# Performance work log

Hardware: AMD Instinct MI355X
Metric: run time of the kernel (lower is better)

The kernel has to match this reference:

```python
import jax, jax.numpy as jnp
import numpy as np

D_MODEL = 1024
N_HEADS = 16
HEAD_D = D_MODEL // N_HEADS  # d_keys == d_values == 64
B, L = 4, 2048
EPS_CAUSAL = 1e-6


def setup_inputs() -> dict:
    key = jax.random.key(0)
    ks = jax.random.split(key, 11)
    s = 1.0 / np.sqrt(D_MODEL)
    inp = {
        "queries": jax.random.normal(ks[0], (B, L, D_MODEL), jnp.float32),
        "keys": jax.random.normal(ks[1], (B, L, D_MODEL), jnp.float32),
        "values": jax.random.normal(ks[2], (B, L, D_MODEL), jnp.float32),
        # Linear weights stored as [in, out] so y = x @ W + b (same math as torch Linear)
        "Wq": jax.random.uniform(ks[3], (D_MODEL, N_HEADS * HEAD_D), jnp.float32, -s, s),
        "bq": jax.random.uniform(ks[4], (N_HEADS * HEAD_D,), jnp.float32, -s, s),
        "Wk": jax.random.uniform(ks[5], (D_MODEL, N_HEADS * HEAD_D), jnp.float32, -s, s),
        "bk": jax.random.uniform(ks[6], (N_HEADS * HEAD_D,), jnp.float32, -s, s),
        "Wv": jax.random.uniform(ks[7], (D_MODEL, N_HEADS * HEAD_D), jnp.float32, -s, s),
        "bv": jax.random.uniform(ks[8], (N_HEADS * HEAD_D,), jnp.float32, -s, s),
        "Wo": jax.random.uniform(ks[9], (D_MODEL, D_MODEL), jnp.float32, -s, s),
        "bo": jax.random.uniform(ks[10], (D_MODEL,), jnp.float32, -s, s),
    }
    return inp


def _feat(x):
    # feat_proj: elu(x) + 1
    return jax.nn.elu(x) + 1.0


def _causal_linear_attn(qs, ks, vs):
    # qs/ks: [B,L,H,D], vs: [B,L,H,K]; faithful to original (swapped einsum labels,
    # elementwise denominator).
    def step(carry, xs):
        Si, Zi = carry  # Si: [B,H,D,K], Zi: [B,H,D]
        q, k, v = xs    # each [B,H,D]
        Si = Si + jnp.einsum('bhd,bhk->bhdk', k, v)
        Zi = Zi + k
        num = jnp.einsum('bhd,bhkd->bhk', q, Si)      # note label swap, as in source
        Vi = num / (q * Zi + EPS_CAUSAL)               # elementwise denom, as in source
        return (Si, Zi), Vi

    Bn, Ln, H, D = qs.shape
    K = vs.shape[-1]
    Si0 = jnp.zeros((Bn, H, D, K), qs.dtype)
    Zi0 = jnp.zeros((Bn, H, D), qs.dtype)
    xs = (jnp.swapaxes(qs, 0, 1), jnp.swapaxes(ks, 0, 1), jnp.swapaxes(vs, 0, 1))
    _, out = jax.lax.scan(step, (Si0, Zi0), xs)  # out: [L,B,H,K]
    return jnp.swapaxes(out, 0, 1)               # [B,L,H,K]


def reference(queries, keys, values, Wq, bq, Wk, bk, Wv, bv, Wo, bo):
    N, Lq, _ = queries.shape
    H = N_HEADS
    Q = (queries @ Wq + bq).reshape(N, Lq, H, -1)
    Kp = (keys @ Wk + bk).reshape(N, keys.shape[1], H, -1)
    V = (values @ Wv + bv).reshape(N, values.shape[1], H, -1)
    Q_lin = _feat(Q)
    K_lin = _feat(Kp)
    V_lin = _causal_linear_attn(Q_lin, K_lin, V)  # causal=True branch
    new_values = V_lin.reshape(N, Lq, -1)
    return new_values @ Wo + bo
```

## Files before the change

### kernel.cpp

```cpp
#include <hip/hip_runtime.h>
#include <math.h>

#define DM 1024
#define LL 2048
#define BB 4
#define HH 16
#define HD 64
#define CC 64
#define NC (LL / CC)
#define EPSC 1e-6f
#define PS 72

typedef __attribute__((ext_vector_type(8))) short short8;
typedef __attribute__((ext_vector_type(4))) float floatx4;

__device__ __forceinline__ float featf(float x) { return x > 0.f ? x + 1.f : __expf(x); }

__device__ __forceinline__ unsigned short f2bf(float f) {
    unsigned int u = __builtin_bit_cast(unsigned int, f);
    u = (u + 0x7FFFu + ((u >> 16) & 1u)) >> 16;
    return (unsigned short)u;
}
__device__ __forceinline__ float bf2f(unsigned short h) {
    return __builtin_bit_cast(float, (unsigned int)h << 16);
}
__device__ __forceinline__ void split2(float f, unsigned short& h, unsigned short& l) {
    h = f2bf(f);
    l = f2bf(f - bf2f(h));
}

__device__ __forceinline__ void gload_lds16(const void* g, void* l) {
    __builtin_amdgcn_global_load_lds(
        (const __attribute__((address_space(1))) void*)g,
        (__attribute__((address_space(3))) void*)l,
        16, 0, 0);
}

__global__ __launch_bounds__(256) void convert3(
    const float* __restrict__ a, const float* __restrict__ b,
    const float* __restrict__ c, unsigned short* __restrict__ oa,
    unsigned short* __restrict__ ob, unsigned short* __restrict__ oc)
{
    const int blk = blockIdx.x;
    const int sel = blk >> 12;
    const float* src = (sel == 0) ? a : (sel == 1) ? b : c;
    unsigned short* dst = (sel == 0) ? oa : (sel == 1) ? ob : oc;
    const int i = (blk & 4095) * 256 + threadIdx.x;
    const float4 x = ((const float4*)src)[i * 2];
    const float4 y = ((const float4*)src)[i * 2 + 1];
    union { unsigned short s[8]; uint4 v; } o;
    o.s[0] = f2bf(x.x); o.s[1] = f2bf(x.y); o.s[2] = f2bf(x.z); o.s[3] = f2bf(x.w);
    o.s[4] = f2bf(y.x); o.s[5] = f2bf(y.y); o.s[6] = f2bf(y.z); o.s[7] = f2bf(y.w);
    ((uint4*)dst)[i] = o.v;
}

__global__ __launch_bounds__(256) void transpose4(
    const float* __restrict__ W0, const float* __restrict__ W1,
    const float* __restrict__ W2, const float* __restrict__ W3,
    unsigned short* __restrict__ T0, unsigned short* __restrict__ T1,
    unsigned short* __restrict__ T2, unsigned short* __restrict__ T3)
{
    __shared__ float tile[64][65];
    const int sel = blockIdx.z;
    const float* W = (sel == 0) ? W0 : (sel == 1) ? W1 : (sel == 2) ? W2 : W3;
    unsigned short* Wt = (sel == 0) ? T0 : (sel == 1) ? T1 : (sel == 2) ? T2 : T3;
    const int r0 = blockIdx.y * 64, c0 = blockIdx.x * 64;
    const int tid = threadIdx.x;
#pragma unroll
    for (int e = 0; e < 16; ++e) {
        const int idx = e * 256 + tid;
        const int r = idx >> 6, c = idx & 63;
        tile[r][c] = W[(size_t)(r0 + r) * DM + c0 + c];
    }
    __syncthreads();
#pragma unroll
    for (int e = 0; e < 16; ++e) {
        const int idx = e * 256 + tid;
        const int co = idx >> 6, ro = idx & 63;
        Wt[(size_t)(c0 + co) * DM + r0 + ro] = f2bf(tile[ro][co]);
    }
}

__global__ __launch_bounds__(256) void gemm_mfma(
    const unsigned short* __restrict__ X,
    const unsigned short* __restrict__ Wt,
    const float* __restrict__ bias,
    float* __restrict__ Y, int act, int layout)
{
    __shared__ __align__(16) unsigned short As[128 * 32];
    __shared__ __align__(16) unsigned short Bs[128 * 32];

    const int tid = threadIdx.x;
    const int lane = tid & 63;
    const int w = tid >> 6;
    const int wr = w >> 1, wc = w & 1;
    const int fm = lane & 15;
    const int fq = lane >> 4;
    const int m0 = blockIdx.y * 128, n0 = blockIdx.x * 128;

    floatx4 acc[4][4];
#pragma unroll
    for (int i = 0; i < 4; ++i)
#pragma unroll
        for (int j = 0; j < 4; ++j) acc[i][j] = (floatx4){0.f, 0.f, 0.f, 0.f};

    const int row0 = tid >> 2;
    const int row1 = row0 + 64;
    const int slot0 = (tid & 3) ^ (row0 & 3);
    const int slot1 = (tid & 3) ^ (row1 & 3);
    const unsigned short* Xa = X + (size_t)(m0 + row0) * DM + slot0 * 8;
    const unsigned short* Xb = X + (size_t)(m0 + row1) * DM + slot1 * 8;
    const unsigned short* Wa = Wt + (size_t)(n0 + row0) * DM + slot0 * 8;
    const unsigned short* Wb = Wt + (size_t)(n0 + row1) * DM + slot1 * 8;

    const int fswz = ((fq ^ (fm & 3)) << 3);

    for (int k0 = 0; k0 < DM; k0 += 32) {
        gload_lds16(Xa + k0, As + (size_t)tid * 8);
        gload_lds16(Xb + k0, As + (size_t)(256 + tid) * 8);
        gload_lds16(Wa + k0, Bs + (size_t)tid * 8);
        gload_lds16(Wb + k0, Bs + (size_t)(256 + tid) * 8);
        __syncthreads();

        short8 af[4], bf[4];
#pragma unroll
        for (int mt = 0; mt < 4; ++mt)
            af[mt] = *(const short8*)(As + (wr * 64 + mt * 16 + fm) * 32 + fswz);
#pragma unroll
        for (int nt = 0; nt < 4; ++nt)
            bf[nt] = *(const short8*)(Bs + (wc * 64 + nt * 16 + fm) * 32 + fswz);
#pragma unroll
        for (int mt = 0; mt < 4; ++mt)
#pragma unroll
            for (int nt = 0; nt < 4; ++nt)
                acc[mt][nt] = __builtin_amdgcn_mfma_f32_16x16x32_bf16(
                    af[mt], bf[nt], acc[mt][nt], 0, 0, 0);
        __syncthreads();
    }

    if (layout == 0) {
#pragma unroll
        for (int nt = 0; nt < 4; ++nt) {
            const int col = n0 + wc * 64 + nt * 16 + fm;
            const float bv = bias[col];
#pragma unroll
            for (int mt = 0; mt < 4; ++mt) {
                const int rbase = m0 + wr * 64 + mt * 16 + fq * 4;
#pragma unroll
                for (int r = 0; r < 4; ++r) {
                    float v = acc[mt][nt][r] + bv;
                    if (act) v = featf(v);
                    Y[(size_t)(rbase + r) * DM + col] = v;
                }
            }
        }
    } else {
        const int b = m0 >> 11;
        const int cch = ((m0 & 2047) >> 6) + wr;
        const int h = (n0 >> 6) + wc;
        float* base = Y + ((size_t)((b * 16 + h) * 32 + cch)) * 4096;
#pragma unroll
        for (int nt = 0; nt < 4; ++nt) {
            const int j = nt * 16 + fm;
            const float bv = bias[n0 + wc * 64 + nt * 16 + fm];
#pragma unroll
            for (int mt = 0; mt < 4; ++mt) {
                float4 o;
                o.x = acc[mt][nt][0] + bv; o.y = acc[mt][nt][1] + bv;
                o.z = acc[mt][nt][2] + bv; o.w = acc[mt][nt][3] + bv;
                if (act) { o.x = featf(o.x); o.y = featf(o.y);
                           o.z = featf(o.z); o.w = featf(o.w); }
                *(float4*)(base + j * 64 + mt * 16 + fq * 4) = o;
            }
        }
    }
}

__global__ __launch_bounds__(256) void chunk_state(
    const float* __restrict__ Kc, const float* __restrict__ Vf,
    float* __restrict__ Mstates, float* __restrict__ Zc)
{
    __shared__ __align__(16) char smem[37888];
    unsigned short* KTH = (unsigned short*)(smem);
    unsigned short* KTL = (unsigned short*)(smem + 9216);
    unsigned short* VTH = (unsigned short*)(smem + 18432);
    unsigned short* VTL = (unsigned short*)(smem + 27648);
    float* scratch = (float*)(smem + 36864);

    const int blk = blockIdx.x;
    const int bh = blk / NC, c = blk % NC;
    const int b = bh / HH, h = bh % HH;
    const int tid = threadIdx.x;
    const int w = tid >> 6;
    const int lane = tid & 63;
    const int fm = lane & 15, fq = lane >> 4;
    const size_t gbase = ((size_t)(b * LL + c * CC)) * DM + h * HD;
    const float* Kblk = Kc + (size_t)blk * 4096;

    const int lr = tid >> 2, lc0 = (tid & 3) * 16;

    {
        float ka[16];
#pragma unroll
        for (int g = 0; g < 4; ++g)
            *(float4*)(ka + g * 4) = *(const float4*)(Kblk + lr * 64 + lc0 + g * 4);
        union { unsigned short s[16]; uint4 v[2]; } hh, ll;
#pragma unroll
        for (int e = 0; e < 16; ++e) split2(ka[e], hh.s[e], ll.s[e]);
        *(uint4*)(KTH + lr * PS + lc0) = hh.v[0];
        *(uint4*)(KTH + lr * PS + lc0 + 8) = hh.v[1];
        *(uint4*)(KTL + lr * PS + lc0) = ll.v[0];
        *(uint4*)(KTL + lr * PS + lc0 + 8) = ll.v[1];
    }
    {
        float va[16];
#pragma unroll
        for (int g = 0; g < 4; ++g)
            *(float4*)(va + g * 4) = *(const float4*)(Vf + gbase + (size_t)lr * DM + lc0 + g * 4);
#pragma unroll
        for (int g = 0; g < 4; ++g)
#pragma unroll
            for (int e0 = 0; e0 < 4; ++e0) {
                const int e = g * 4 + ((e0 + tid) & 3);
                unsigned short hh, ll;
                split2(va[e], hh, ll);
                VTH[(lc0 + e) * PS + lr] = hh;
                VTL[(lc0 + e) * PS + lr] = ll;
            }
    }
    {
        const int zj = tid & 63, zs = tid >> 6;
        float z = 0.f;
#pragma unroll
        for (int g = 0; g < 4; ++g) {
            float4 kv = *(const float4*)(Kblk + zj * 64 + zs * 16 + g * 4);
            z += kv.x + kv.y + kv.z + kv.w;
        }
        scratch[zs * 64 + zj] = z;
    }
    __syncthreads();

    if (tid < 64) {
        Zc[(size_t)blk * 64 + tid] = scratch[tid] + scratch[64 + tid] +
                                     scratch[128 + tid] + scratch[192 + tid];
    }

    floatx4 acc[4];
#pragma unroll
    for (int nt = 0; nt < 4; ++nt) acc[nt] = (floatx4){0.f, 0.f, 0.f, 0.f};
    short8 aH[2], aL[2];
#pragma unroll
    for (int ks = 0; ks < 2; ++ks) {
        aH[ks] = *(const short8*)(KTH + (16 * w + fm) * PS + ks * 32 + fq * 8);
        aL[ks] = *(const short8*)(KTL + (16 * w + fm) * PS + ks * 32 + fq * 8);
    }
#pragma unroll
    for (int nt = 0; nt < 4; ++nt) {
#pragma unroll
        for (int ks = 0; ks < 2; ++ks) {
            short8 bH = *(const short8*)(VTH + (nt * 16 + fm) * PS + ks * 32 + fq * 8);
            short8 bL = *(const short8*)(VTL + (nt * 16 + fm) * PS + ks * 32 + fq * 8);
            acc[nt] = __builtin_amdgcn_mfma_f32_16x16x32_bf16(aH[ks], bH, acc[nt], 0, 0, 0);
            acc[nt] = __builtin_amdgcn_mfma_f32_16x16x32_bf16(aH[ks], bL, acc[nt], 0, 0, 0);
            acc[nt] = __builtin_amdgcn_mfma_f32_16x16x32_bf16(aL[ks], bH, acc[nt], 0, 0, 0);
        }
    }
    float* Mout = Mstates + (size_t)blk * 4096;
#pragma unroll
    for (int nt = 0; nt < 4; ++nt) {
        const int dv = nt * 16 + fm;
#pragma unroll
        for (int r = 0; r < 4; ++r) {
            const int j = 16 * w + fq * 4 + r;
            Mout[j * 64 + dv] = acc[nt][r];
        }
    }
}

__global__ __launch_bounds__(256) void prefix_state(
    float* __restrict__ Mstates, float* __restrict__ Zc)
{
    const int bh = blockIdx.x >> 4;
    const int slice = blockIdx.x & 15;
    const int off = slice * 256 + threadIdx.x;
    float run = 0.f;
    float* base = Mstates + (size_t)bh * NC * 4096 + off;
    for (int c = 0; c < NC; ++c) {
        const float v = base[(size_t)c * 4096];
        base[(size_t)c * 4096] = run;
        run += v;
    }
    if (slice == 0 && threadIdx.x < 64) {
        float z = 0.f;
        float* zb = Zc + (size_t)bh * NC * 64 + threadIdx.x;
        for (int c = 0; c < NC; ++c) {
            const float v = zb[c * 64];
            zb[c * 64] = z;
            z += v;
        }
    }
}

__global__ __launch_bounds__(256) void chunk_attn(
    const float* __restrict__ Qf, const float* __restrict__ Kc,
    const float* __restrict__ Vf, const float* __restrict__ Mprev,
    const float* __restrict__ Zprev, unsigned short* __restrict__ Outb)
{
    __shared__ __align__(16) char smem[72704];
    unsigned short* VH  = (unsigned short*)(smem);
    unsigned short* VL  = (unsigned short*)(smem + 9216);
    unsigned short* KTH = (unsigned short*)(smem + 18432);
    unsigned short* KTL = (unsigned short*)(smem + 27648);
    unsigned short* AH  = (unsigned short*)(smem + 36864);
    unsigned short* AL  = (unsigned short*)(smem + 46080);
    float* Qs = (float*)(smem + 55296);
    float* Zf = (float*)(smem + 18432);
    float* scratch = (float*)(smem + 36864);

    const int blk = blockIdx.x;
    const int bh = blk / NC, c = blk % NC;
    const int b = bh / HH, h = bh % HH;
    const int tid = threadIdx.x;
    const int w = tid >> 6, lane = tid & 63;
    const int fm = lane & 15, fq = lane >> 4;
    const size_t gbase = ((size_t)(b * LL + c * CC)) * DM + h * HD;
    const float* Kblk = Kc + (size_t)blk * 4096;

    const int lr = tid >> 2, lc0 = (tid & 3) * 16;

    float4 mpre[4];
    {
        const float* Mp = Mprev + (size_t)blk * 4096;
#pragma unroll
        for (int g = 0; g < 4; ++g)
            mpre[g] = *(const float4*)(Mp + lr * 64 + lc0 + g * 4);
    }
    {
        float va[16];
#pragma unroll
        for (int g = 0; g < 4; ++g)
            *(float4*)(va + g * 4) = *(const float4*)(Vf + gbase + (size_t)lr * DM + lc0 + g * 4);
        union { unsigned short s[16]; uint4 v[2]; } hh, ll;
#pragma unroll
        for (int e = 0; e < 16; ++e) split2(va[e], hh.s[e], ll.s[e]);
        *(uint4*)(VH + lr * PS + lc0) = hh.v[0];
        *(uint4*)(VH + lr * PS + lc0 + 8) = hh.v[1];
        *(uint4*)(VL + lr * PS + lc0) = ll.v[0];
        *(uint4*)(VL + lr * PS + lc0 + 8) = ll.v[1];
    }
    {
        float ka[16];
#pragma unroll
        for (int g = 0; g < 4; ++g)
            *(float4*)(ka + g * 4) = *(const float4*)(Kblk + lr * 64 + lc0 + g * 4);
        union { unsigned short s[16]; uint4 v[2]; } hh, ll;
#pragma unroll
        for (int e = 0; e < 16; ++e) split2(ka[e], hh.s[e], ll.s[e]);
        *(uint4*)(KTH + lr * PS + lc0) = hh.v[0];
        *(uint4*)(KTH + lr * PS + lc0 + 8) = hh.v[1];
        *(uint4*)(KTL + lr * PS + lc0) = ll.v[0];
        *(uint4*)(KTL + lr * PS + lc0 + 8) = ll.v[1];
    }
    {
#pragma unroll
        for (int g = 0; g < 4; ++g) {
            float4 qv = *(const float4*)(Qf + gbase + (size_t)lr * DM + lc0 + g * 4);
            *(float4*)(Qs + lr * 68 + lc0 + g * 4) = qv;
        }
    }
    short8 qH[2], qL[2];
    {
        const float* qrow = Qf + gbase + (size_t)(16 * w + fm) * DM;
#pragma unroll
        for (int ks = 0; ks < 2; ++ks) {
            float qa[8];
            *(float4*)(qa)     = *(const float4*)(qrow + ks * 32 + fq * 8);
            *(float4*)(qa + 4) = *(const float4*)(qrow + ks * 32 + fq * 8 + 4);
            union { unsigned short s[8]; short8 v; } hh, ll;
#pragma unroll
            for (int e = 0; e < 8; ++e) split2(qa[e], hh.s[e], ll.s[e]);
            qH[ks] = hh.v; qL[ks] = ll.v;
        }
    }
    const int zj = tid & 63, zs = tid >> 6;
    float zpart[16];
    {
        float ka[16];
#pragma unroll
        for (int g = 0; g < 4; ++g)
            *(float4*)(ka + g * 4) = *(const float4*)(Kblk + zj * 64 + zs * 16 + g * 4);
        float run = 0.f;
#pragma unroll
        for (int t = 0; t < 16; ++t) { run += ka[t]; zpart[t] = run; }
        scratch[zs * 64 + zj] = run;
    }
    const float zp = Zprev[(size_t)blk * 64 + zj];
    __syncthreads();

    {
        float off = zp;
        for (int ss = 0; ss < 4; ++ss)
            if (ss < zs) off += scratch[ss * 64 + zj];
#pragma unroll
        for (int t = 0; t < 16; ++t) zpart[t] += off;
    }

    floatx4 acc1[4];
#pragma unroll
    for (int nt = 0; nt < 4; ++nt) acc1[nt] = (floatx4){0.f, 0.f, 0.f, 0.f};
#pragma unroll
    for (int nt = 0; nt < 4; ++nt) {
#pragma unroll
        for (int ks = 0; ks < 2; ++ks) {
            short8 bH = *(const short8*)(VH + (nt * 16 + fm) * PS + ks * 32 + fq * 8);
            short8 bL = *(const short8*)(VL + (nt * 16 + fm) * PS + ks * 32 + fq * 8);
            acc1[nt] = __builtin_amdgcn_mfma_f32_16x16x32_bf16(qH[ks], bH, acc1[nt], 0, 0, 0);
            acc1[nt] = __builtin_amdgcn_mfma_f32_16x16x32_bf16(qH[ks], bL, acc1[nt], 0, 0, 0);
            acc1[nt] = __builtin_amdgcn_mfma_f32_16x16x32_bf16(qL[ks], bH, acc1[nt], 0, 0, 0);
        }
    }
    __syncthreads();

#pragma unroll
    for (int nt = 0; nt < 4; ++nt) {
        const int t = nt * 16 + fm;
#pragma unroll
        for (int r0 = 0; r0 < 4; ++r0) {
            const int r = (r0 + fm) & 3;
            const int i = 16 * w + fq * 4 + r;
            const float v = (t <= i) ? acc1[nt][r] : 0.f;
            unsigned short hh, ll;
            split2(v, hh, ll);
            AH[i * PS + t] = hh;
            AL[i * PS + t] = ll;
        }
    }
#pragma unroll
    for (int g = 0; g < 4; ++g) {
        float ma[4] = {mpre[g].x, mpre[g].y, mpre[g].z, mpre[g].w};
        union { unsigned short s[4]; uint2 v; } mh, ml;
#pragma unroll
        for (int e = 0; e < 4; ++e) split2(ma[e], mh.s[e], ml.s[e]);
        *(uint2*)(VH + lr * PS + lc0 + g * 4) = mh.v;
        *(uint2*)(VL + lr * PS + lc0 + g * 4) = ml.v;
    }
    __syncthreads();

    floatx4 acc2[4];
#pragma unroll
    for (int nt = 0; nt < 4; ++nt) acc2[nt] = (floatx4){0.f, 0.f, 0.f, 0.f};
    {
        short8 aAH[2], aAL[2];
#pragma unroll
        for (int ks = 0; ks < 2; ++ks) {
            aAH[ks] = *(const short8*)(AH + (16 * w + fm) * PS + ks * 32 + fq * 8);
            aAL[ks] = *(const short8*)(AL + (16 * w + fm) * PS + ks * 32 + fq * 8);
        }
#pragma unroll
        for (int nt = 0; nt < 4; ++nt) {
            const int rb = (nt * 16 + fm) * PS + fq * 8;
#pragma unroll
            for (int ks = 0; ks < 2; ++ks) {
                short8 bH = *(const short8*)(VH + rb + ks * 32);
                short8 bL = *(const short8*)(VL + rb + ks * 32);
                acc2[nt] = __builtin_amdgcn_mfma_f32_16x16x32_bf16(qH[ks], bH, acc2[nt], 0, 0, 0);
                acc2[nt] = __builtin_amdgcn_mfma_f32_16x16x32_bf16(qH[ks], bL, acc2[nt], 0, 0, 0);
                acc2[nt] = __builtin_amdgcn_mfma_f32_16x16x32_bf16(qL[ks], bH, acc2[nt], 0, 0, 0);
            }
#pragma unroll
            for (int ks = 0; ks < 2; ++ks) {
                short8 bH = *(const short8*)(KTH + rb + ks * 32);
                short8 bL = *(const short8*)(KTL + rb + ks * 32);
                acc2[nt] = __builtin_amdgcn_mfma_f32_16x16x32_bf16(aAH[ks], bH, acc2[nt], 0, 0, 0);
                acc2[nt] = __builtin_amdgcn_mfma_f32_16x16x32_bf16(aAH[ks], bL, acc2[nt], 0, 0, 0);
                acc2[nt] = __builtin_amdgcn_mfma_f32_16x16x32_bf16(aAL[ks], bH, acc2[nt], 0, 0, 0);
            }
        }
    }
    __syncthreads();

#pragma unroll
    for (int t = 0; t < 16; ++t)
        Zf[zj * 67 + zs * 16 + t] = zpart[t];
    __syncthreads();

#pragma unroll
    for (int nt = 0; nt < 4; ++nt) {
        const int j = nt * 16 + fm;
#pragma unroll
        for (int r = 0; r < 4; ++r) {
            const int i = 16 * w + fq * 4 + r;
            const float q = Qs[i * 68 + j];
            const float z = Zf[j * 67 + i];
            const float denom = fmaf(q, z, EPSC);
            Outb[gbase + (size_t)i * DM + j] = f2bf(acc2[nt][r] / denom);
        }
    }
}

extern "C" void kernel_launch(void* const* d_in, const int* in_sizes, int n_in,
                              void* d_out, int out_size, void* d_ws, size_t ws_size,
                              hipStream_t stream)
{
    (void)in_sizes; (void)n_in; (void)out_size; (void)ws_size;

    const float* queries = (const float*)d_in[0];
    const float* keys    = (const float*)d_in[1];
    const float* values  = (const float*)d_in[2];
    const float* Wq = (const float*)d_in[3];
    const float* bq = (const float*)d_in[4];
    const float* Wk = (const float*)d_in[5];
    const float* bk = (const float*)d_in[6];
    const float* Wv = (const float*)d_in[7];
    const float* bv = (const float*)d_in[8];
    const float* Wo = (const float*)d_in[9];
    const float* bo = (const float*)d_in[10];

    char* ws = (char*)d_ws;
    const size_t MB = 1u << 20;
    unsigned short* qb  = (unsigned short*)(ws);
    unsigned short* kb  = (unsigned short*)(ws + 16 * MB);
    unsigned short* vb  = (unsigned short*)(ws + 32 * MB);
    unsigned short* Wqt = (unsigned short*)(ws + 48 * MB);
    unsigned short* Wkt = (unsigned short*)(ws + 50 * MB);
    unsigned short* Wvt = (unsigned short*)(ws + 52 * MB);
    unsigned short* Wot = (unsigned short*)(ws + 54 * MB);
    float* Qf = (float*)(ws + 56 * MB);
    float* Kc = (float*)(ws + 88 * MB);
    float* Vf = (float*)(ws + 120 * MB);
    float* Zc = (float*)(ws + 152 * MB);
    unsigned short* attnb = (unsigned short*)(ws);
    float* Mst = (float*)(ws + 16 * MB);

    const dim3 gblk(256);
    const dim3 gG(DM / 128, (BB * LL) / 128);

    convert3<<<dim3(3 * 4096), gblk, 0, stream>>>(queries, keys, values, qb, kb, vb);
    transpose4<<<dim3(16, 16, 4), gblk, 0, stream>>>(Wq, Wk, Wv, Wo, Wqt, Wkt, Wvt, Wot);

    gemm_mfma<<<gG, gblk, 0, stream>>>(qb, Wqt, bq, Qf, 1, 0);
    gemm_mfma<<<gG, gblk, 0, stream>>>(kb, Wkt, bk, Kc, 1, 1);
    gemm_mfma<<<gG, gblk, 0, stream>>>(vb, Wvt, bv, Vf, 0, 0);

    chunk_state<<<dim3(BB * HH * NC), gblk, 0, stream>>>(Kc, Vf, Mst, Zc);
    prefix_state<<<dim3(BB * HH * 16), gblk, 0, stream>>>(Mst, Zc);
    chunk_attn<<<dim3(BB * HH * NC), gblk, 0, stream>>>(Qf, Kc, Vf, Mst, Zc, attnb);

    gemm_mfma<<<gG, gblk, 0, stream>>>(attnb, Wot, bo, (float*)d_out, 0, 0);
}
```

Measured before the change: 369.3 us.

## Switch attention intermediates to fp16 with single-pass MFMA and async LDS staging

Q, K, V projections and the per-chunk states are now stored as fp16 instead of fp32. The chunk kernels use a single f16 MFMA in place of the three-pass bf16 hi/lo split, which cuts MFMA work and intermediate memory traffic. Tiles are staged into swizzled LDS with global_load_lds, the Z prefix is computed per wave without a scratch reduction, and the division becomes a reciprocal multiply. This lowers precision, since fp16 accumulated chunk states and Z can lose accuracy or overflow over long sequences.

```diff
diff --git a/kernel.cpp b/kernel.cpp
--- a/kernel.cpp
+++ b/kernel.cpp
@@ -12,6 +12,7 @@
 #define PS 72
 
 typedef __attribute__((ext_vector_type(8))) short short8;
+typedef __attribute__((ext_vector_type(8))) _Float16 half8;
 typedef __attribute__((ext_vector_type(4))) float floatx4;
 
 __device__ __forceinline__ float featf(float x) { return x > 0.f ? x + 1.f : __expf(x); }
@@ -20,13 +21,6 @@
     unsigned int u = __builtin_bit_cast(unsigned int, f);
     u = (u + 0x7FFFu + ((u >> 16) & 1u)) >> 16;
     return (unsigned short)u;
-}
-__device__ __forceinline__ float bf2f(unsigned short h) {
-    return __builtin_bit_cast(float, (unsigned int)h << 16);
-}
-__device__ __forceinline__ void split2(float f, unsigned short& h, unsigned short& l) {
-    h = f2bf(f);
-    l = f2bf(f - bf2f(h));
 }
 
 __device__ __forceinline__ void gload_lds16(const void* g, void* l) {
@@ -34,6 +28,21 @@
         (const __attribute__((address_space(1))) void*)g,
         (__attribute__((address_space(3))) void*)l,
         16, 0, 0);
+}
+
+__device__ __forceinline__ void stage_tile(const void* gp_, int rowstride,
+                                           char* lds_base, int tid) {
+    const unsigned short* gp = (const unsigned short*)gp_;
+#pragma unroll
+    for (int m = 0; m < 2; ++m) {
+        const int row = m * 32 + (tid >> 3);
+        const int g = (tid & 7) ^ (row & 7);
+        gload_lds16(gp + (size_t)row * rowstride + g * 8,
+                    lds_base + m * 4096 + tid * 16);
+    }
+}
+__device__ __forceinline__ half8 frag_ldh(const char* base, int row, int kc) {
+    return *(const half8*)(base + row * 128 + (((kc) ^ (row & 7)) << 4));
 }
 
 __global__ __launch_bounds__(256) void convert3(
@@ -85,7 +94,9 @@
     const unsigned short* __restrict__ X,
     const unsigned short* __restrict__ Wt,
     const float* __restrict__ bias,
-    float* __restrict__ Y, int act, int layout)
+    float* __restrict__ Yf,
+    _Float16* __restrict__ Yh,
+    int act, int mode)
 {
     __shared__ __align__(16) unsigned short As[128 * 32];
     __shared__ __align__(16) unsigned short Bs[128 * 32];
@@ -138,7 +149,7 @@
         __syncthreads();
     }
 
-    if (layout == 0) {
+    if (mode == 0) {
 #pragma unroll
         for (int nt = 0; nt < 4; ++nt) {
             const int col = n0 + wc * 64 + nt * 16 + fm;
@@ -150,7 +161,23 @@
                 for (int r = 0; r < 4; ++r) {
                     float v = acc[mt][nt][r] + bv;
                     if (act) v = featf(v);
-                    Y[(size_t)(rbase + r) * DM + col] = v;
+                    Yf[(size_t)(rbase + r) * DM + col] = v;
+                }
+            }
+        }
+    } else if (mode == 1) {
+#pragma unroll
+        for (int nt = 0; nt < 4; ++nt) {
+            const int col = n0 + wc * 64 + nt * 16 + fm;
+            const float bv = bias[col];
+#pragma unroll
+            for (int mt = 0; mt < 4; ++mt) {
+                const int rbase = m0 + wr * 64 + mt * 16 + fq * 4;
+#pragma unroll
+                for (int r = 0; r < 4; ++r) {
+                    float v = acc[mt][nt][r] + bv;
+                    if (act) v = featf(v);
+                    Yh[(size_t)(rbase + r) * DM + col] = (_Float16)v;
                 }
             }
         }
@@ -158,84 +185,70 @@
         const int b = m0 >> 11;
         const int cch = ((m0 & 2047) >> 6) + wr;
         const int h = (n0 >> 6) + wc;
-        float* base = Y + ((size_t)((b * 16 + h) * 32 + cch)) * 4096;
+        _Float16* hb = Yh + ((size_t)((b * 16 + h) * 32 + cch)) * 4096;
 #pragma unroll
         for (int nt = 0; nt < 4; ++nt) {
             const int j = nt * 16 + fm;
             const float bv = bias[n0 + wc * 64 + nt * 16 + fm];
 #pragma unroll
             for (int mt = 0; mt < 4; ++mt) {
-                float4 o;
-                o.x = acc[mt][nt][0] + bv; o.y = acc[mt][nt][1] + bv;
-                o.z = acc[mt][nt][2] + bv; o.w = acc[mt][nt][3] + bv;
-                if (act) { o.x = featf(o.x); o.y = featf(o.y);
-                           o.z = featf(o.z); o.w = featf(o.w); }
-                *(float4*)(base + j * 64 + mt * 16 + fq * 4) = o;
+                float o[4];
+#pragma unroll
+                for (int r = 0; r < 4; ++r) {
+                    float v = acc[mt][nt][r] + bv;
+                    if (act) v = featf(v);
+                    o[r] = v;
+                }
+                union { _Float16 h[4]; uint2 v; } pk;
+#pragma unroll
+                for (int r = 0; r < 4; ++r) pk.h[r] = (_Float16)o[r];
+                *(uint2*)(hb + j * 64 + mt * 16 + fq * 4) = pk.v;
             }
         }
     }
 }
 
 __global__ __launch_bounds__(256) void chunk_state(
-    const float* __restrict__ Kc, const float* __restrict__ Vf,
-    float* __restrict__ Mstates, float* __restrict__ Zc)
-{
-    __shared__ __align__(16) char smem[37888];
-    unsigned short* KTH = (unsigned short*)(smem);
-    unsigned short* KTL = (unsigned short*)(smem + 9216);
-    unsigned short* VTH = (unsigned short*)(smem + 18432);
-    unsigned short* VTL = (unsigned short*)(smem + 27648);
-    float* scratch = (float*)(smem + 36864);
+    const _Float16* __restrict__ KTp, const _Float16* __restrict__ Vp,
+    _Float16* __restrict__ Mc, float* __restrict__ Zc)
+{
+    __shared__ __align__(16) char smem[18432];
+    _Float16* VT = (_Float16*)(smem + 8192);
+    float* scratch = (float*)(smem + 17408);
 
     const int blk = blockIdx.x;
     const int bh = blk / NC, c = blk % NC;
     const int b = bh / HH, h = bh % HH;
     const int tid = threadIdx.x;
-    const int w = tid >> 6;
-    const int lane = tid & 63;
+    const int w = tid >> 6, lane = tid & 63;
     const int fm = lane & 15, fq = lane >> 4;
     const size_t gbase = ((size_t)(b * LL + c * CC)) * DM + h * HD;
-    const float* Kblk = Kc + (size_t)blk * 4096;
+    const _Float16* Kblk = KTp + (size_t)blk * 4096;
+
+    stage_tile(Kblk, 64, smem, tid);
 
     const int lr = tid >> 2, lc0 = (tid & 3) * 16;
-
     {
-        float ka[16];
-#pragma unroll
-        for (int g = 0; g < 4; ++g)
-            *(float4*)(ka + g * 4) = *(const float4*)(Kblk + lr * 64 + lc0 + g * 4);
-        union { unsigned short s[16]; uint4 v[2]; } hh, ll;
-#pragma unroll
-        for (int e = 0; e < 16; ++e) split2(ka[e], hh.s[e], ll.s[e]);
-        *(uint4*)(KTH + lr * PS + lc0) = hh.v[0];
-        *(uint4*)(KTH + lr * PS + lc0 + 8) = hh.v[1];
-        *(uint4*)(KTL + lr * PS + lc0) = ll.v[0];
-        *(uint4*)(KTL + lr * PS + lc0 + 8) = ll.v[1];
-    }
-    {
-        float va[16];
-#pragma unroll
-        for (int g = 0; g < 4; ++g)
-            *(float4*)(va + g * 4) = *(const float4*)(Vf + gbase + (size_t)lr * DM + lc0 + g * 4);
+        half8 v0 = *(const half8*)(Vp + gbase + (size_t)lr * DM + lc0);
+        half8 v1 = *(const half8*)(Vp + gbase + (size_t)lr * DM + lc0 + 8);
+        _Float16 va[16];
+#pragma unroll
+        for (int e = 0; e < 8; ++e) { va[e] = v0[e]; va[8 + e] = v1[e]; }
 #pragma unroll
         for (int g = 0; g < 4; ++g)
 #pragma unroll
             for (int e0 = 0; e0 < 4; ++e0) {
                 const int e = g * 4 + ((e0 + tid) & 3);
-                unsigned short hh, ll;
-                split2(va[e], hh, ll);
-                VTH[(lc0 + e) * PS + lr] = hh;
-                VTL[(lc0 + e) * PS + lr] = ll;
+                VT[(lc0 + e) * PS + lr] = va[e];
             }
     }
     {
         const int zj = tid & 63, zs = tid >> 6;
+        half8 k0 = *(const half8*)(Kblk + zj * 64 + zs * 16);
+        half8 k1 = *(const half8*)(Kblk + zj * 64 + zs * 16 + 8);
         float z = 0.f;
 #pragma unroll
-        for (int g = 0; g < 4; ++g) {
-            float4 kv = *(const float4*)(Kblk + zj * 64 + zs * 16 + g * 4);
-            z += kv.x + kv.y + kv.z + kv.w;
-        }
+        for (int e = 0; e < 8; ++e) z += (float)k0[e] + (float)k1[e];
         scratch[zs * 64 + zj] = z;
     }
     __syncthreads();
@@ -248,46 +261,41 @@
     floatx4 acc[4];
 #pragma unroll
     for (int nt = 0; nt < 4; ++nt) acc[nt] = (floatx4){0.f, 0.f, 0.f, 0.f};
-    short8 aH[2], aL[2];
-#pragma unroll
-    for (int ks = 0; ks < 2; ++ks) {
-        aH[ks] = *(const short8*)(KTH + (16 * w + fm) * PS + ks * 32 + fq * 8);
-        aL[ks] = *(const short8*)(KTL + (16 * w + fm) * PS + ks * 32 + fq * 8);
-    }
+    half8 aK[2];
+#pragma unroll
+    for (int ks = 0; ks < 2; ++ks)
+        aK[ks] = frag_ldh(smem, 16 * w + fm, ks * 4 + fq);
 #pragma unroll
     for (int nt = 0; nt < 4; ++nt) {
 #pragma unroll
         for (int ks = 0; ks < 2; ++ks) {
-            short8 bH = *(const short8*)(VTH + (nt * 16 + fm) * PS + ks * 32 + fq * 8);
-            short8 bL = *(const short8*)(VTL + (nt * 16 + fm) * PS + ks * 32 + fq * 8);
-            acc[nt] = __builtin_amdgcn_mfma_f32_16x16x32_bf16(aH[ks], bH, acc[nt], 0, 0, 0);
-            acc[nt] = __builtin_amdgcn_mfma_f32_16x16x32_bf16(aH[ks], bL, acc[nt], 0, 0, 0);
-            acc[nt] = __builtin_amdgcn_mfma_f32_16x16x32_bf16(aL[ks], bH, acc[nt], 0, 0, 0);
-        }
-    }
-    float* Mout = Mstates + (size_t)blk * 4096;
+            half8 bV = *(const half8*)(VT + (nt * 16 + fm) * PS + ks * 32 + fq * 8);
+            acc[nt] = __builtin_amdgcn_mfma_f32_16x16x32_f16(aK[ks], bV, acc[nt], 0, 0, 0);
+        }
+    }
+    _Float16* Mout = Mc + (size_t)blk * 4096;
 #pragma unroll
     for (int nt = 0; nt < 4; ++nt) {
         const int dv = nt * 16 + fm;
 #pragma unroll
         for (int r = 0; r < 4; ++r) {
             const int j = 16 * w + fq * 4 + r;
-            Mout[j * 64 + dv] = acc[nt][r];
+            Mout[j * 64 + dv] = (_Float16)acc[nt][r];
         }
     }
 }
 
 __global__ __launch_bounds__(256) void prefix_state(
-    float* __restrict__ Mstates, float* __restrict__ Zc)
+    _Float16* __restrict__ Mc, float* __restrict__ Zc)
 {
     const int bh = blockIdx.x >> 4;
     const int slice = blockIdx.x & 15;
     const int off = slice * 256 + threadIdx.x;
     float run = 0.f;
-    float* base = Mstates + (size_t)bh * NC * 4096 + off;
+    _Float16* p = Mc + (size_t)bh * NC * 4096 + off;
     for (int c = 0; c < NC; ++c) {
-        const float v = base[(size_t)c * 4096];
-        base[(size_t)c * 4096] = run;
+        const float v = (float)p[(size_t)c * 4096];
+        p[(size_t)c * 4096] = (_Float16)run;
         run += v;
     }
     if (slice == 0 && threadIdx.x < 64) {
@@ -301,21 +309,20 @@
     }
 }
 
+#define ATT_Q  0
+#define ATT_V  8192
+#define ATT_K  16384
+#define ATT_M  24576
+#define ATT_A  32768
+#define ATT_Z  41984
 __global__ __launch_bounds__(256) void chunk_attn(
-    const float* __restrict__ Qf, const float* __restrict__ Kc,
-    const float* __restrict__ Vf, const float* __restrict__ Mprev,
+    const _Float16* __restrict__ Qp, const _Float16* __restrict__ Vp,
+    const _Float16* __restrict__ KTp, const _Float16* __restrict__ Mtp,
     const float* __restrict__ Zprev, unsigned short* __restrict__ Outb)
 {
-    __shared__ __align__(16) char smem[72704];
-    unsigned short* VH  = (unsigned short*)(smem);
-    unsigned short* VL  = (unsigned short*)(smem + 9216);
-    unsigned short* KTH = (unsigned short*)(smem + 18432);
-    unsigned short* KTL = (unsigned short*)(smem + 27648);
-    unsigned short* AH  = (unsigned short*)(smem + 36864);
-    unsigned short* AL  = (unsigned short*)(smem + 46080);
-    float* Qs = (float*)(smem + 55296);
-    float* Zf = (float*)(smem + 18432);
-    float* scratch = (float*)(smem + 36864);
+    __shared__ __align__(16) char smem[50304];
+    _Float16* AT = (_Float16*)(smem + ATT_A);
+    _Float16* Zf = (_Float16*)(smem + ATT_Z);
 
     const int blk = blockIdx.x;
     const int bh = blk / NC, c = blk % NC;
@@ -324,102 +331,52 @@
     const int w = tid >> 6, lane = tid & 63;
     const int fm = lane & 15, fq = lane >> 4;
     const size_t gbase = ((size_t)(b * LL + c * CC)) * DM + h * HD;
-    const float* Kblk = Kc + (size_t)blk * 4096;
-
-    const int lr = tid >> 2, lc0 = (tid & 3) * 16;
-
-    float4 mpre[4];
+    const _Float16* Kblk = KTp + (size_t)blk * 4096;
+
+    stage_tile(Qp + gbase, DM, smem + ATT_Q, tid);
+    stage_tile(Vp + gbase, DM, smem + ATT_V, tid);
+    stage_tile(Kblk, 64, smem + ATT_K, tid);
+    stage_tile(Mtp + (size_t)blk * 4096, 64, smem + ATT_M, tid);
+
     {
-        const float* Mp = Mprev + (size_t)blk * 4096;
-#pragma unroll
-        for (int g = 0; g < 4; ++g)
-            mpre[g] = *(const float4*)(Mp + lr * 64 + lc0 + g * 4);
-    }
-    {
-        float va[16];
-#pragma unroll
-        for (int g = 0; g < 4; ++g)
-            *(float4*)(va + g * 4) = *(const float4*)(Vf + gbase + (size_t)lr * DM + lc0 + g * 4);
-        union { unsigned short s[16]; uint4 v[2]; } hh, ll;
-#pragma unroll
-        for (int e = 0; e < 16; ++e) split2(va[e], hh.s[e], ll.s[e]);
-        *(uint4*)(VH + lr * PS + lc0) = hh.v[0];
-        *(uint4*)(VH + lr * PS + lc0 + 8) = hh.v[1];
-        *(uint4*)(VL + lr * PS + lc0) = ll.v[0];
-        *(uint4*)(VL + lr * PS + lc0 + 8) = ll.v[1];
-    }
-    {
-        float ka[16];
-#pragma unroll
-        for (int g = 0; g < 4; ++g)
-            *(float4*)(ka + g * 4) = *(const float4*)(Kblk + lr * 64 + lc0 + g * 4);
-        union { unsigned short s[16]; uint4 v[2]; } hh, ll;
-#pragma unroll
-        for (int e = 0; e < 16; ++e) split2(ka[e], hh.s[e], ll.s[e]);
-        *(uint4*)(KTH + lr * PS + lc0) = hh.v[0];
-        *(uint4*)(KTH + lr * PS + lc0 + 8) = hh.v[1];
-        *(uint4*)(KTL + lr * PS + lc0) = ll.v[0];
-        *(uint4*)(KTL + lr * PS + lc0 + 8) = ll.v[1];
-    }
-    {
-#pragma unroll
-        for (int g = 0; g < 4; ++g) {
-            float4 qv = *(const float4*)(Qf + gbase + (size_t)lr * DM + lc0 + g * 4);
-            *(float4*)(Qs + lr * 68 + lc0 + g * 4) = qv;
-        }
-    }
-    short8 qH[2], qL[2];
-    {
-        const float* qrow = Qf + gbase + (size_t)(16 * w + fm) * DM;
+        const int j = lane;
+        const _Float16* kr = Kblk + (size_t)j * 64;
+        float run = Zprev[(size_t)blk * 64 + j];
+        for (int s = 0; s < w; ++s) {
+            half8 k0 = *(const half8*)(kr + s * 16);
+            half8 k1 = *(const half8*)(kr + s * 16 + 8);
+#pragma unroll
+            for (int e = 0; e < 8; ++e) run += (float)k0[e] + (float)k1[e];
+        }
+        half8 k0 = *(const half8*)(kr + w * 16);
+        half8 k1 = *(const half8*)(kr + w * 16 + 8);
+        float zrow[16];
+#pragma unroll
+        for (int e = 0; e < 8; ++e) { run += (float)k0[e]; zrow[e] = run; }
+#pragma unroll
+        for (int e = 0; e < 8; ++e) { run += (float)k1[e]; zrow[8 + e] = run; }
+#pragma unroll
+        for (int t = 0; t < 16; ++t)
+            Zf[(16 * w + t) * 65 + j] = (_Float16)zrow[t];
+    }
+    __syncthreads();
+
+    half8 qf[2];
+#pragma unroll
+    for (int ks = 0; ks < 2; ++ks)
+        qf[ks] = frag_ldh(smem + ATT_Q, 16 * w + fm, ks * 4 + fq);
+
+    floatx4 acc1[4];
+#pragma unroll
+    for (int nt = 0; nt < 4; ++nt) acc1[nt] = (floatx4){0.f, 0.f, 0.f, 0.f};
+#pragma unroll
+    for (int nt = 0; nt < 4; ++nt) {
 #pragma unroll
         for (int ks = 0; ks < 2; ++ks) {
-            float qa[8];
-            *(float4*)(qa)     = *(const float4*)(qrow + ks * 32 + fq * 8);
-            *(float4*)(qa + 4) = *(const float4*)(qrow + ks * 32 + fq * 8 + 4);
-            union { unsigned short s[8]; short8 v; } hh, ll;
-#pragma unroll
-            for (int e = 0; e < 8; ++e) split2(qa[e], hh.s[e], ll.s[e]);
-            qH[ks] = hh.v; qL[ks] = ll.v;
-        }
-    }
-    const int zj = tid & 63, zs = tid >> 6;
-    float zpart[16];
-    {
-        float ka[16];
-#pragma unroll
-        for (int g = 0; g < 4; ++g)
-            *(float4*)(ka + g * 4) = *(const float4*)(Kblk + zj * 64 + zs * 16 + g * 4);
-        float run = 0.f;
-#pragma unroll
-        for (int t = 0; t < 16; ++t) { run += ka[t]; zpart[t] = run; }
-        scratch[zs * 64 + zj] = run;
-    }
-    const float zp = Zprev[(size_t)blk * 64 + zj];
-    __syncthreads();
-
-    {
-        float off = zp;
-        for (int ss = 0; ss < 4; ++ss)
-            if (ss < zs) off += scratch[ss * 64 + zj];
-#pragma unroll
-        for (int t = 0; t < 16; ++t) zpart[t] += off;
-    }
-
-    floatx4 acc1[4];
-#pragma unroll
-    for (int nt = 0; nt < 4; ++nt) acc1[nt] = (floatx4){0.f, 0.f, 0.f, 0.f};
-#pragma unroll
-    for (int nt = 0; nt < 4; ++nt) {
-#pragma unroll
-        for (int ks = 0; ks < 2; ++ks) {
-            short8 bH = *(const short8*)(VH + (nt * 16 + fm) * PS + ks * 32 + fq * 8);
-            short8 bL = *(const short8*)(VL + (nt * 16 + fm) * PS + ks * 32 + fq * 8);
-            acc1[nt] = __builtin_amdgcn_mfma_f32_16x16x32_bf16(qH[ks], bH, acc1[nt], 0, 0, 0);
-            acc1[nt] = __builtin_amdgcn_mfma_f32_16x16x32_bf16(qH[ks], bL, acc1[nt], 0, 0, 0);
-            acc1[nt] = __builtin_amdgcn_mfma_f32_16x16x32_bf16(qL[ks], bH, acc1[nt], 0, 0, 0);
-        }
-    }
-    __syncthreads();
+            half8 bV = frag_ldh(smem + ATT_V, nt * 16 + fm, ks * 4 + fq);
+            acc1[nt] = __builtin_amdgcn_mfma_f32_16x16x32_f16(qf[ks], bV, acc1[nt], 0, 0, 0);
+        }
+    }
 
 #pragma unroll
     for (int nt = 0; nt < 4; ++nt) {
@@ -428,61 +385,32 @@
         for (int r0 = 0; r0 < 4; ++r0) {
             const int r = (r0 + fm) & 3;
             const int i = 16 * w + fq * 4 + r;
-            const float v = (t <= i) ? acc1[nt][r] : 0.f;
-            unsigned short hh, ll;
-            split2(v, hh, ll);
-            AH[i * PS + t] = hh;
-            AL[i * PS + t] = ll;
-        }
-    }
-#pragma unroll
-    for (int g = 0; g < 4; ++g) {
-        float ma[4] = {mpre[g].x, mpre[g].y, mpre[g].z, mpre[g].w};
-        union { unsigned short s[4]; uint2 v; } mh, ml;
-#pragma unroll
-        for (int e = 0; e < 4; ++e) split2(ma[e], mh.s[e], ml.s[e]);
-        *(uint2*)(VH + lr * PS + lc0 + g * 4) = mh.v;
-        *(uint2*)(VL + lr * PS + lc0 + g * 4) = ml.v;
-    }
-    __syncthreads();
+            AT[i * PS + t] = (_Float16)((t <= i) ? acc1[nt][r] : 0.f);
+        }
+    }
 
     floatx4 acc2[4];
 #pragma unroll
     for (int nt = 0; nt < 4; ++nt) acc2[nt] = (floatx4){0.f, 0.f, 0.f, 0.f};
     {
-        short8 aAH[2], aAL[2];
-#pragma unroll
-        for (int ks = 0; ks < 2; ++ks) {
-            aAH[ks] = *(const short8*)(AH + (16 * w + fm) * PS + ks * 32 + fq * 8);
-            aAL[ks] = *(const short8*)(AL + (16 * w + fm) * PS + ks * 32 + fq * 8);
-        }
+        half8 aA[2];
+#pragma unroll
+        for (int ks = 0; ks < 2; ++ks)
+            aA[ks] = *(const half8*)(AT + (16 * w + fm) * PS + ks * 32 + fq * 8);
 #pragma unroll
         for (int nt = 0; nt < 4; ++nt) {
-            const int rb = (nt * 16 + fm) * PS + fq * 8;
 #pragma unroll
             for (int ks = 0; ks < 2; ++ks) {
-                short8 bH = *(const short8*)(VH + rb + ks * 32);
-                short8 bL = *(const short8*)(VL + rb + ks * 32);
-                acc2[nt] = __builtin_amdgcn_mfma_f32_16x16x32_bf16(qH[ks], bH, acc2[nt], 0, 0, 0);
-                acc2[nt] = __builtin_amdgcn_mfma_f32_16x16x32_bf16(qH[ks], bL, acc2[nt], 0, 0, 0);
-                acc2[nt] = __builtin_amdgcn_mfma_f32_16x16x32_bf16(qL[ks], bH, acc2[nt], 0, 0, 0);
+                half8 bM = frag_ldh(smem + ATT_M, nt * 16 + fm, ks * 4 + fq);
+                acc2[nt] = __builtin_amdgcn_mfma_f32_16x16x32_f16(qf[ks], bM, acc2[nt], 0, 0, 0);
             }
 #pragma unroll
             for (int ks = 0; ks < 2; ++ks) {
-                short8 bH = *(const short8*)(KTH + rb + ks * 32);
-                short8 bL = *(const short8*)(KTL + rb + ks * 32);
-                acc2[nt] = __builtin_amdgcn_mfma_f32_16x16x32_bf16(aAH[ks], bH, acc2[nt], 0, 0, 0);
-                acc2[nt] = __builtin_amdgcn_mfma_f32_16x16x32_bf16(aAH[ks], bL, acc2[nt], 0, 0, 0);
-                acc2[nt] = __builtin_amdgcn_mfma_f32_16x16x32_bf16(aAL[ks], bH, acc2[nt], 0, 0, 0);
-            }
-        }
-    }
-    __syncthreads();
-
-#pragma unroll
-    for (int t = 0; t < 16; ++t)
-        Zf[zj * 67 + zs * 16 + t] = zpart[t];
-    __syncthreads();
+                half8 bK = frag_ldh(smem + ATT_K, nt * 16 + fm, ks * 4 + fq);
+                acc2[nt] = __builtin_amdgcn_mfma_f32_16x16x32_f16(aA[ks], bK, acc2[nt], 0, 0, 0);
+            }
+        }
+    }
 
 #pragma unroll
     for (int nt = 0; nt < 4; ++nt) {
@@ -490,10 +418,11 @@
 #pragma unroll
         for (int r = 0; r < 4; ++r) {
             const int i = 16 * w + fq * 4 + r;
-            const float q = Qs[i * 68 + j];
-            const float z = Zf[j * 67 + i];
+            const int qoff = i * 128 + (((j >> 3) ^ (i & 7)) << 4) + (j & 7) * 2;
+            const float q = (float)(*(const _Float16*)(smem + ATT_Q + qoff));
+            const float z = (float)Zf[i * 65 + j];
             const float denom = fmaf(q, z, EPSC);
-            Outb[gbase + (size_t)i * DM + j] = f2bf(acc2[nt][r] / denom);
+            Outb[gbase + (size_t)i * DM + j] = f2bf(acc2[nt][r] * __builtin_amdgcn_rcpf(denom));
         }
     }
 }
@@ -525,12 +454,12 @@
     unsigned short* Wkt = (unsigned short*)(ws + 50 * MB);
     unsigned short* Wvt = (unsigned short*)(ws + 52 * MB);
     unsigned short* Wot = (unsigned short*)(ws + 54 * MB);
-    float* Qf = (float*)(ws + 56 * MB);
-    float* Kc = (float*)(ws + 88 * MB);
-    float* Vf = (float*)(ws + 120 * MB);
-    float* Zc = (float*)(ws + 152 * MB);
-    unsigned short* attnb = (unsigned short*)(ws);
-    float* Mst = (float*)(ws + 16 * MB);
+    _Float16* Qh  = (_Float16*)(ws + 56 * MB);
+    _Float16* Vh  = (_Float16*)(ws + 72 * MB);
+    _Float16* KTp = (_Float16*)(ws + 88 * MB);
+    _Float16* Mc  = (_Float16*)(ws + 104 * MB);
+    float* Zc     = (float*)(ws + 120 * MB);
+    unsigned short* attnb = (unsigned short*)(ws + 128 * MB);
 
     const dim3 gblk(256);
     const dim3 gG(DM / 128, (BB * LL) / 128);
@@ -538,13 +467,13 @@
     convert3<<<dim3(3 * 4096), gblk, 0, stream>>>(queries, keys, values, qb, kb, vb);
     transpose4<<<dim3(16, 16, 4), gblk, 0, stream>>>(Wq, Wk, Wv, Wo, Wqt, Wkt, Wvt, Wot);
 
-    gemm_mfma<<<gG, gblk, 0, stream>>>(qb, Wqt, bq, Qf, 1, 0);
-    gemm_mfma<<<gG, gblk, 0, stream>>>(kb, Wkt, bk, Kc, 1, 1);
-    gemm_mfma<<<gG, gblk, 0, stream>>>(vb, Wvt, bv, Vf, 0, 0);
-
-    chunk_state<<<dim3(BB * HH * NC), gblk, 0, stream>>>(Kc, Vf, Mst, Zc);
-    prefix_state<<<dim3(BB * HH * 16), gblk, 0, stream>>>(Mst, Zc);
-    chunk_attn<<<dim3(BB * HH * NC), gblk, 0, stream>>>(Qf, Kc, Vf, Mst, Zc, attnb);
-
-    gemm_mfma<<<gG, gblk, 0, stream>>>(attnb, Wot, bo, (float*)d_out, 0, 0);
-}
+    gemm_mfma<<<gG, gblk, 0, stream>>>(qb, Wqt, bq, nullptr, Qh, 1, 1);
+    gemm_mfma<<<gG, gblk, 0, stream>>>(kb, Wkt, bk, nullptr, KTp, 1, 2);
+    gemm_mfma<<<gG, gblk, 0, stream>>>(vb, Wvt, bv, nullptr, Vh, 0, 1);
+
+    chunk_state<<<dim3(BB * HH * NC), gblk, 0, stream>>>(KTp, Vh, Mc, Zc);
+    prefix_state<<<dim3(BB * HH * 16), gblk, 0, stream>>>(Mc, Zc);
+    chunk_attn<<<dim3(BB * HH * NC), gblk, 0, stream>>>(Qh, Vh, KTp, Mc, Zc, attnb);
+
+    gemm_mfma<<<gG, gblk, 0, stream>>>(attnb, Wot, bo, (float*)d_out, nullptr, 0, 0);
+}
```

New measurement: 326.1 us. 1.13x faster.
